# Optimization experiments

Hardware: AMD Instinct MI355X
Metric: run time of the kernel (lower is better)

The kernel has to match this reference:

```python
import jax, jax.numpy as jnp
import numpy as np

CONTEXT_LENGTH = 4096
INPUT_LENGTH = 1024
N_EMBED = 512
HEAD_SIZE = 64
BATCH = 8


def _prefix_causal_mask(T):
    # A=ones(IL,IL), B=zeros(IL,non), C=ones(non,IL), D=tril(non,non)
    il = INPUT_LENGTH
    non = CONTEXT_LENGTH - il
    top = jnp.concatenate([jnp.ones((il, il)), jnp.zeros((il, non))], axis=1)
    bot = jnp.concatenate([jnp.ones((non, il)), jnp.tril(jnp.ones((non, non)))], axis=1)
    E = jnp.concatenate([top, bot], axis=0)
    return E[:T, :T]


def setup_inputs() -> dict:
    key = jax.random.key(0)
    kx, kq, kk, kv = jax.random.split(key, 4)
    scale = N_EMBED ** -0.5
    return {
        "x": jax.random.normal(kx, (BATCH, CONTEXT_LENGTH, N_EMBED), dtype=jnp.float32),
        "Wq": jax.random.normal(kq, (N_EMBED, HEAD_SIZE), dtype=jnp.float32) * scale,
        "Wk": jax.random.normal(kk, (N_EMBED, HEAD_SIZE), dtype=jnp.float32) * scale,
        "Wv": jax.random.normal(kv, (N_EMBED, HEAD_SIZE), dtype=jnp.float32) * scale,
    }


def reference(x, Wq, Wk, Wv):
    B, T, C = x.shape
    q = x @ Wq  # [B,T,h]
    k = x @ Wk  # [B,T,h]
    v = x @ Wv  # [B,T,h]
    # NOTE: original scales by C**-0.5 with C = n_embed (not head_size)
    wei = jnp.einsum("bth,bsh->bts", q, k) * (C ** -0.5)  # [B,T,T]
    mask = _prefix_causal_mask(T)  # [T,T], 1 = visible
    wei = jnp.where(mask == 0, jnp.float32(-jnp.inf), wei)
    wei = jax.nn.softmax(wei, axis=-1)
    # dropout p=0.0 (eval): identity
    return jnp.einsum("bts,bsh->bth", wei, v)  # [B,T,h]
```

## Files before the change

### kernel.cpp

```cpp
#include <hip/hip_runtime.h>
#include <hip/hip_bf16.h>


typedef short short8 __attribute__((ext_vector_type(8)));
typedef float floatx4 __attribute__((ext_vector_type(4)));

static __device__ __forceinline__ unsigned short f2b(float f) {
  unsigned u = __float_as_uint(f);
  unsigned r = (u + 0x7fffu + ((u >> 16) & 1u)) >> 16;
  return (unsigned short)r;
}

static __device__ __forceinline__ unsigned pkbf(float lo, float hi) {
  __hip_bfloat162 t = __float22bfloat162_rn(make_float2(lo, hi));
  unsigned d;
  __builtin_memcpy(&d, &t, 4);
  return d;
}

union S8U {
  short8 s;
  unsigned u[4];
};

__global__ __launch_bounds__(256) void wtrans(
    const float* __restrict__ Wq, const float* __restrict__ Wk,
    const float* __restrict__ Wv, unsigned short* __restrict__ Wtf) {
  int o = blockIdx.x * 256 + threadIdx.x;
  int e = o & 7;
  int ln = (o >> 3) & 63;
  int jg = o >> 9;
  int ks = jg / 12;
  int j = jg % 12;
  int m = j >> 2;
  int n = (j & 3) * 16 + (ln & 15);
  int k = ks * 32 + (ln >> 4) * 8 + e;
  const float* W = (m == 0) ? Wq : (m == 1) ? Wk : Wv;
  Wtf[o] = f2b(W[k * 64 + n]);
}

__global__ __launch_bounds__(256, 3) void proj(
    const float* __restrict__ x, const unsigned short* __restrict__ Wtf,
    unsigned short* __restrict__ q, unsigned short* __restrict__ Kf,
    unsigned short* __restrict__ Vf) {
  __shared__ float Cc[2][12][16][17];

  const int tid = threadIdx.x;
  const int lane = tid & 63;
  const int w = tid >> 6;
  const int u = lane & 15;
  const int qd = lane >> 4;
  const int pr = w >> 1;
  const int p = w & 1;
  const int g0 = blockIdx.x * 32;

  floatx4 acc[12];
#pragma unroll
  for (int j = 0; j < 12; ++j) acc[j] = (floatx4)0.0f;

  const float* xr = x + (size_t)(g0 + pr * 16 + u) * 512;

  for (int it = 0; it < 8; ++it) {
    const int ks = p + it * 2;
    floatx4 x0 = *reinterpret_cast<const floatx4*>(&xr[ks * 32 + qd * 8]);
    floatx4 x1 = *reinterpret_cast<const floatx4*>(&xr[ks * 32 + qd * 8 + 4]);
    S8U a;
    a.u[0] = pkbf(x0[0], x0[1]);
    a.u[1] = pkbf(x0[2], x0[3]);
    a.u[2] = pkbf(x1[0], x1[1]);
    a.u[3] = pkbf(x1[2], x1[3]);
#pragma unroll
    for (int j = 0; j < 12; ++j) {
      short8 bfr = *reinterpret_cast<const short8*>(&Wtf[(size_t)(ks * 12 + j) * 512 + lane * 8]);
      acc[j] = __builtin_amdgcn_mfma_f32_16x16x32_bf16(a.s, bfr, acc[j], 0, 0, 0);
    }
  }

  if (p == 1) {
#pragma unroll
    for (int j = 0; j < 12; ++j)
#pragma unroll
      for (int r = 0; r < 4; ++r)
        Cc[pr][j][qd * 4 + r][u] = acc[j][r];
  }
  __syncthreads();
  if (p == 0) {
#pragma unroll
    for (int j = 0; j < 12; ++j)
#pragma unroll
      for (int r = 0; r < 4; ++r)
        acc[j][r] += Cc[pr][j][qd * 4 + r][u];

    const int rbase = g0 + pr * 16;
    const int b = rbase >> 12;
    const int t = rbase & 4095;
    const int kt = t >> 6;
    const int sb = ((blockIdx.x & 1) << 1) + pr;
    const int sp = blockIdx.x & 1;
    unsigned short* kfb = Kf + ((size_t)(b * 64 + kt)) * 4096;
    unsigned short* vfb = Vf + ((size_t)(b * 64 + kt)) * 4096;

#pragma unroll
    for (int j = 0; j < 4; ++j)
#pragma unroll
      for (int r = 0; r < 4; ++r) {
        q[(size_t)(rbase + qd * 4 + r) * 64 + j * 16 + u] = f2b(acc[j][r]);
        {
          int kh = j >> 1;
          int qd_f = ((j & 1) << 1) + (u >> 3);
          kfb[(size_t)(kh * 4 + sb) * 512 + (qd_f * 16 + (qd * 4 + r)) * 8 + (u & 7)] =
              f2b(acc[4 + j][r]);
        }
        {
          int qd_f = pr * 2 + (qd >> 1);
          int e = ((qd & 1) << 2) + r;
          vfb[(size_t)(sp * 4 + j) * 512 + (qd_f * 16 + u) * 8 + e] = f2b(acc[8 + j][r]);
        }
      }
  }
}

__global__ __launch_bounds__(256, 2) void attn(
    const unsigned short* __restrict__ q, const unsigned short* __restrict__ Kf,
    const unsigned short* __restrict__ Vf, float* __restrict__ out) {
  __shared__ unsigned Pb[4][4][64][4];
  __shared__ float OcA[64][68];
  __shared__ float OcB[64][68];
  __shared__ float Lc[4][64];

  const int tid = threadIdx.x;
  const int lane = tid & 63;
  const int w = tid >> 6;
  const int u = lane & 15;
  const int qd = lane >> 4;

  const int bx = blockIdx.x;
  const int b = bx & 7;
  const int i = bx >> 3;
  const int qt = (i < 32) ? i : (95 - i);
  const int g0 = qt * 64;

  const unsigned short* qp = q + (size_t)b * 4096 * 64;
  const unsigned short* kfp = Kf + (size_t)b * 64 * 4096;
  const unsigned short* vfp = Vf + (size_t)b * 64 * 4096;

  short8 qB[4][2];
#pragma unroll
  for (int nb = 0; nb < 4; ++nb)
#pragma unroll
    for (int kh = 0; kh < 2; ++kh)
      qB[nb][kh] = *reinterpret_cast<const short8*>(
          &qp[(size_t)(g0 + nb * 16 + u) * 64 + kh * 32 + qd * 8]);

  floatx4 OT[4][4];
#pragma unroll
  for (int mb = 0; mb < 4; ++mb)
#pragma unroll
    for (int nb = 0; nb < 4; ++nb) OT[mb][nb] = (floatx4)0.0f;
  float L[4] = {0.f, 0.f, 0.f, 0.f};

  const float cexp = 0.04419417382415922f * 1.4426950408889634f;
  const int ktmax = (qt < 16) ? 15 : qt;

  for (int kt = w; kt <= ktmax; kt += 4) {
    const unsigned short* kb = kfp + (size_t)kt * 4096;
    const unsigned short* vb = vfp + (size_t)kt * 4096;
    short8 kA[8];
#pragma unroll
    for (int f = 0; f < 8; ++f)
      kA[f] = *reinterpret_cast<const short8*>(&kb[(size_t)f * 512 + lane * 8]);
    const bool diag = (qt >= 16) && (kt == qt);

#pragma unroll
    for (int sp = 0; sp < 2; ++sp) {
      short8 vA[4];
#pragma unroll
      for (int mb = 0; mb < 4; ++mb)
        vA[mb] = *reinterpret_cast<const short8*>(
            &vb[(size_t)(sp * 4 + mb) * 512 + lane * 8]);

      floatx4 ST[2][4];
#pragma unroll
      for (int sbb = 0; sbb < 2; ++sbb)
#pragma unroll
        for (int nb = 0; nb < 4; ++nb) ST[sbb][nb] = (floatx4)0.0f;
#pragma unroll
      for (int kh = 0; kh < 2; ++kh)
#pragma unroll
        for (int sbb = 0; sbb < 2; ++sbb)
#pragma unroll
          for (int nb = 0; nb < 4; ++nb)
            ST[sbb][nb] = __builtin_amdgcn_mfma_f32_16x16x32_bf16(
                kA[kh * 4 + sp * 2 + sbb], qB[nb][kh], ST[sbb][nb], 0, 0, 0);

      if (diag) {
#pragma unroll
        for (int sbb = 0; sbb < 2; ++sbb)
#pragma unroll
          for (int nb = 0; nb < 4; ++nb)
#pragma unroll
            for (int r = 0; r < 4; ++r) {
              int sl = (sp * 2 + sbb) * 16 + qd * 4 + r;
              int qr = nb * 16 + u;
              if (sl > qr) ST[sbb][nb][r] = -__builtin_inff();
            }
      }

#pragma unroll
      for (int sbb = 0; sbb < 2; ++sbb)
#pragma unroll
        for (int nb = 0; nb < 4; ++nb) {
#pragma unroll
          for (int r = 0; r < 4; ++r)
            ST[sbb][nb][r] = __builtin_amdgcn_exp2f(ST[sbb][nb][r] * cexp);
          L[nb] += (ST[sbb][nb][0] + ST[sbb][nb][1]) + (ST[sbb][nb][2] + ST[sbb][nb][3]);
          unsigned lo = pkbf(ST[sbb][nb][0], ST[sbb][nb][1]);
          unsigned hi = pkbf(ST[sbb][nb][2], ST[sbb][nb][3]);
          int dl = (sbb * 2 + (qd >> 1)) * 16 + u;
          int d0 = (qd & 1) * 2;
          *reinterpret_cast<uint2*>(&Pb[w][nb][dl][d0]) = make_uint2(lo, hi);
        }

#pragma unroll
      for (int nb = 0; nb < 4; ++nb) {
        short8 pB = *reinterpret_cast<const short8*>(&Pb[w][nb][lane][0]);
#pragma unroll
        for (int mb = 0; mb < 4; ++mb)
          OT[mb][nb] = __builtin_amdgcn_mfma_f32_16x16x32_bf16(vA[mb], pB, OT[mb][nb], 0, 0, 0);
      }
    }
  }

#pragma unroll
  for (int nb = 0; nb < 4; ++nb) {
    L[nb] += __shfl_xor(L[nb], 16);
    L[nb] += __shfl_xor(L[nb], 32);
  }
  if (lane < 16) {
#pragma unroll
    for (int nb = 0; nb < 4; ++nb) Lc[w][nb * 16 + lane] = L[nb];
  }

  if (w == 1) {
#pragma unroll
    for (int mb = 0; mb < 4; ++mb)
#pragma unroll
      for (int nb = 0; nb < 4; ++nb)
        *reinterpret_cast<floatx4*>(&OcA[nb * 16 + u][mb * 16 + qd * 4]) = OT[mb][nb];
  }
  if (w == 3) {
#pragma unroll
    for (int mb = 0; mb < 4; ++mb)
#pragma unroll
      for (int nb = 0; nb < 4; ++nb)
        *reinterpret_cast<floatx4*>(&OcB[nb * 16 + u][mb * 16 + qd * 4]) = OT[mb][nb];
  }
  __syncthreads();
  if (w == 0) {
#pragma unroll
    for (int mb = 0; mb < 4; ++mb)
#pragma unroll
      for (int nb = 0; nb < 4; ++nb)
        OT[mb][nb] += *reinterpret_cast<const floatx4*>(&OcA[nb * 16 + u][mb * 16 + qd * 4]);
  }
  if (w == 2) {
#pragma unroll
    for (int mb = 0; mb < 4; ++mb)
#pragma unroll
      for (int nb = 0; nb < 4; ++nb) {
        OT[mb][nb] += *reinterpret_cast<const floatx4*>(&OcB[nb * 16 + u][mb * 16 + qd * 4]);
        *reinterpret_cast<floatx4*>(&OcB[nb * 16 + u][mb * 16 + qd * 4]) = OT[mb][nb];
      }
  }
  __syncthreads();
  if (w == 0) {
#pragma unroll
    for (int mb = 0; mb < 4; ++mb)
#pragma unroll
      for (int nb = 0; nb < 4; ++nb) {
        OT[mb][nb] += *reinterpret_cast<const floatx4*>(&OcB[nb * 16 + u][mb * 16 + qd * 4]);
        *reinterpret_cast<floatx4*>(&OcA[nb * 16 + u][mb * 16 + qd * 4]) = OT[mb][nb];
      }
  }
  __syncthreads();

  {
    int qr = tid >> 2;
    int h0 = (tid & 3) * 16;
    float Ltot = (Lc[0][qr] + Lc[1][qr]) + (Lc[2][qr] + Lc[3][qr]);
    float inv = 1.0f / Ltot;
    float* op = out + ((size_t)b * 4096 + g0 + qr) * 64 + h0;
#pragma unroll
    for (int c = 0; c < 4; ++c) {
      floatx4 v = *reinterpret_cast<const floatx4*>(&OcA[qr][h0 + c * 4]);
      v *= inv;
      *reinterpret_cast<floatx4*>(&op[c * 4]) = v;
    }
  }
}

extern "C" void kernel_launch(void* const* d_in, const int* in_sizes, int n_in,
                              void* d_out, int out_size, void* d_ws, size_t ws_size,
                              hipStream_t stream) {
  const float* x  = (const float*)d_in[0];
  const float* Wq = (const float*)d_in[1];
  const float* Wk = (const float*)d_in[2];
  const float* Wv = (const float*)d_in[3];

  unsigned short* ws = (unsigned short*)d_ws;
  unsigned short* Wtf = ws;
  unsigned short* qb = ws + 131072;
  unsigned short* kf = qb + 2097152;
  unsigned short* vf = kf + 2097152;

  wtrans<<<384, 256, 0, stream>>>(Wq, Wk, Wv, Wtf);
  proj<<<1024, 256, 0, stream>>>(x, Wtf, qb, kf, vf);
  attn<<<512, 256, 0, stream>>>(qb, kf, vf, (float*)d_out);
}
```

Before: 146.8 us.

## Split-K balance attention work across blocks with partial outputs and fold kernel

Replaces per-query-tile block assignment with a flat partition of all (query tile, key tile) work units so each block processes an equal number of key tiles, possibly spanning query-tile boundaries. Each block writes unnormalized partial outputs and row sums to workspace, and a new fold kernel sums the partials and normalizes. The softmax scale is also folded into q during projection, which removes a multiply per score. In exchange it adds an extra kernel launch and extra global traffic for the fp32 partials.

New measurement: 153.0 us. +4.3%, slower.

```diff
diff --git a/kernel.cpp b/kernel.cpp
--- a/kernel.cpp
+++ b/kernel.cpp
@@ -91,6 +91,7 @@
       for (int r = 0; r < 4; ++r)
         acc[j][r] += Cc[pr][j][qd * 4 + r][u];
 
+    const float cexp = 0.04419417382415922f * 1.4426950408889634f;
     const int rbase = g0 + pr * 16;
     const int b = rbase >> 12;
     const int t = rbase & 4095;
@@ -104,7 +105,7 @@
     for (int j = 0; j < 4; ++j)
 #pragma unroll
       for (int r = 0; r < 4; ++r) {
-        q[(size_t)(rbase + qd * 4 + r) * 64 + j * 16 + u] = f2b(acc[j][r]);
+        q[(size_t)(rbase + qd * 4 + r) * 64 + j * 16 + u] = f2b(acc[j][r] * cexp);
         {
           int kh = j >> 1;
           int qd_f = ((j & 1) << 1) + (u >> 3);
@@ -122,7 +123,8 @@
 
 __global__ __launch_bounds__(256, 2) void attn(
     const unsigned short* __restrict__ q, const unsigned short* __restrict__ Kf,
-    const unsigned short* __restrict__ Vf, float* __restrict__ out) {
+    const unsigned short* __restrict__ Vf, float* __restrict__ Op,
+    float* __restrict__ Lp) {
   __shared__ unsigned Pb[4][4][64][4];
   __shared__ float OcA[64][68];
   __shared__ float OcB[64][68];
@@ -136,166 +138,229 @@
 
   const int bx = blockIdx.x;
   const int b = bx & 7;
-  const int i = bx >> 3;
-  const int qt = (i < 32) ? i : (95 - i);
-  const int g0 = qt * 64;
+  const int s = bx >> 3;
+
+  const int ts = (s * 2200) >> 6;
+  const int te = ((s + 1) * 2200) >> 6;
 
   const unsigned short* qp = q + (size_t)b * 4096 * 64;
   const unsigned short* kfp = Kf + (size_t)b * 64 * 4096;
   const unsigned short* vfp = Vf + (size_t)b * 64 * 4096;
 
-  short8 qB[4][2];
-#pragma unroll
-  for (int nb = 0; nb < 4; ++nb)
-#pragma unroll
-    for (int kh = 0; kh < 2; ++kh)
-      qB[nb][kh] = *reinterpret_cast<const short8*>(
-          &qp[(size_t)(g0 + nb * 16 + u) * 64 + kh * 32 + qd * 8]);
-
-  floatx4 OT[4][4];
-#pragma unroll
-  for (int mb = 0; mb < 4; ++mb)
-#pragma unroll
-    for (int nb = 0; nb < 4; ++nb) OT[mb][nb] = (floatx4)0.0f;
-  float L[4] = {0.f, 0.f, 0.f, 0.f};
-
-  const float cexp = 0.04419417382415922f * 1.4426950408889634f;
-  const int ktmax = (qt < 16) ? 15 : qt;
-
-  for (int kt = w; kt <= ktmax; kt += 4) {
-    const unsigned short* kb = kfp + (size_t)kt * 4096;
-    const unsigned short* vb = vfp + (size_t)kt * 4096;
-    short8 kA[8];
-#pragma unroll
-    for (int f = 0; f < 8; ++f)
-      kA[f] = *reinterpret_cast<const short8*>(&kb[(size_t)f * 512 + lane * 8]);
-    const bool diag = (qt >= 16) && (kt == qt);
-
-#pragma unroll
-    for (int sp = 0; sp < 2; ++sp) {
-      short8 vA[4];
-#pragma unroll
-      for (int mb = 0; mb < 4; ++mb)
-        vA[mb] = *reinterpret_cast<const short8*>(
-            &vb[(size_t)(sp * 4 + mb) * 512 + lane * 8]);
-
-      floatx4 ST[2][4];
-#pragma unroll
-      for (int sbb = 0; sbb < 2; ++sbb)
-#pragma unroll
-        for (int nb = 0; nb < 4; ++nb) ST[sbb][nb] = (floatx4)0.0f;
+  int qt = 0, cq = 0;
+  while (cq + ((qt < 16) ? 16 : (qt + 1)) <= ts) {
+    cq += (qt < 16) ? 16 : (qt + 1);
+    ++qt;
+  }
+
+  int tcur = ts;
+  while (tcur < te) {
+    const int tq = (qt < 16) ? 16 : (qt + 1);
+    const int a = tcur - cq;
+    const int bnd = (tq < te - cq) ? tq : (te - cq);
+    int k0 = (cq * 64) / 2200;
+    while ((((k0 + 1) * 2200) >> 6) <= cq) ++k0;
+    const int o = s - k0;
+    const int g0 = qt * 64;
+    const int diagkt = (qt >= 16) ? qt : -1;
+
+    short8 qB[4][2];
+#pragma unroll
+    for (int nb = 0; nb < 4; ++nb)
 #pragma unroll
       for (int kh = 0; kh < 2; ++kh)
+        qB[nb][kh] = *reinterpret_cast<const short8*>(
+            &qp[(size_t)(g0 + nb * 16 + u) * 64 + kh * 32 + qd * 8]);
+
+    floatx4 OT[4][4];
+#pragma unroll
+    for (int mb = 0; mb < 4; ++mb)
+#pragma unroll
+      for (int nb = 0; nb < 4; ++nb) OT[mb][nb] = (floatx4)0.0f;
+    float L[4] = {0.f, 0.f, 0.f, 0.f};
+
+    for (int kt = a + w; kt < bnd; kt += 4) {
+      const unsigned short* kb = kfp + (size_t)kt * 4096;
+      const unsigned short* vb = vfp + (size_t)kt * 4096;
+      short8 kA[8];
+#pragma unroll
+      for (int f = 0; f < 8; ++f)
+        kA[f] = *reinterpret_cast<const short8*>(&kb[(size_t)f * 512 + lane * 8]);
+      const bool diag = (kt == diagkt);
+
+#pragma unroll
+      for (int sp = 0; sp < 2; ++sp) {
+        short8 vA[4];
+#pragma unroll
+        for (int mb = 0; mb < 4; ++mb)
+          vA[mb] = *reinterpret_cast<const short8*>(
+              &vb[(size_t)(sp * 4 + mb) * 512 + lane * 8]);
+
+        floatx4 ST[2][4];
 #pragma unroll
         for (int sbb = 0; sbb < 2; ++sbb)
 #pragma unroll
-          for (int nb = 0; nb < 4; ++nb)
-            ST[sbb][nb] = __builtin_amdgcn_mfma_f32_16x16x32_bf16(
-                kA[kh * 4 + sp * 2 + sbb], qB[nb][kh], ST[sbb][nb], 0, 0, 0);
-
-      if (diag) {
+          for (int nb = 0; nb < 4; ++nb) ST[sbb][nb] = (floatx4)0.0f;
+#pragma unroll
+        for (int kh = 0; kh < 2; ++kh)
+#pragma unroll
+          for (int sbb = 0; sbb < 2; ++sbb)
+#pragma unroll
+            for (int nb = 0; nb < 4; ++nb)
+              ST[sbb][nb] = __builtin_amdgcn_mfma_f32_16x16x32_bf16(
+                  kA[kh * 4 + sp * 2 + sbb], qB[nb][kh], ST[sbb][nb], 0, 0, 0);
+
+        if (diag) {
+#pragma unroll
+          for (int sbb = 0; sbb < 2; ++sbb)
+#pragma unroll
+            for (int nb = 0; nb < 4; ++nb)
+#pragma unroll
+              for (int r = 0; r < 4; ++r) {
+                int sl = (sp * 2 + sbb) * 16 + qd * 4 + r;
+                int qr = nb * 16 + u;
+                if (sl > qr) ST[sbb][nb][r] = -__builtin_inff();
+              }
+        }
+
 #pragma unroll
         for (int sbb = 0; sbb < 2; ++sbb)
 #pragma unroll
-          for (int nb = 0; nb < 4; ++nb)
-#pragma unroll
-            for (int r = 0; r < 4; ++r) {
-              int sl = (sp * 2 + sbb) * 16 + qd * 4 + r;
-              int qr = nb * 16 + u;
-              if (sl > qr) ST[sbb][nb][r] = -__builtin_inff();
-            }
+          for (int nb = 0; nb < 4; ++nb) {
+#pragma unroll
+            for (int r = 0; r < 4; ++r)
+              ST[sbb][nb][r] = __builtin_amdgcn_exp2f(ST[sbb][nb][r]);
+            L[nb] += (ST[sbb][nb][0] + ST[sbb][nb][1]) + (ST[sbb][nb][2] + ST[sbb][nb][3]);
+            unsigned lo = pkbf(ST[sbb][nb][0], ST[sbb][nb][1]);
+            unsigned hi = pkbf(ST[sbb][nb][2], ST[sbb][nb][3]);
+            int dl = (sbb * 2 + (qd >> 1)) * 16 + u;
+            int d0 = (qd & 1) * 2;
+            *reinterpret_cast<uint2*>(&Pb[w][nb][dl][d0]) = make_uint2(lo, hi);
+          }
+
+#pragma unroll
+        for (int nb = 0; nb < 4; ++nb) {
+          short8 pB = *reinterpret_cast<const short8*>(&Pb[w][nb][lane][0]);
+#pragma unroll
+          for (int mb = 0; mb < 4; ++mb)
+            OT[mb][nb] = __builtin_amdgcn_mfma_f32_16x16x32_bf16(vA[mb], pB, OT[mb][nb], 0, 0, 0);
+        }
       }
-
-#pragma unroll
-      for (int sbb = 0; sbb < 2; ++sbb)
+    }
+
+#pragma unroll
+    for (int nb = 0; nb < 4; ++nb) {
+      L[nb] += __shfl_xor(L[nb], 16);
+      L[nb] += __shfl_xor(L[nb], 32);
+    }
+    if (lane < 16) {
+#pragma unroll
+      for (int nb = 0; nb < 4; ++nb) Lc[w][nb * 16 + lane] = L[nb];
+    }
+
+    if (w == 1) {
+#pragma unroll
+      for (int mb = 0; mb < 4; ++mb)
+#pragma unroll
+        for (int nb = 0; nb < 4; ++nb)
+          *reinterpret_cast<floatx4*>(&OcA[nb * 16 + u][mb * 16 + qd * 4]) = OT[mb][nb];
+    }
+    if (w == 3) {
+#pragma unroll
+      for (int mb = 0; mb < 4; ++mb)
+#pragma unroll
+        for (int nb = 0; nb < 4; ++nb)
+          *reinterpret_cast<floatx4*>(&OcB[nb * 16 + u][mb * 16 + qd * 4]) = OT[mb][nb];
+    }
+    __syncthreads();
+    if (w == 0) {
+#pragma unroll
+      for (int mb = 0; mb < 4; ++mb)
+#pragma unroll
+        for (int nb = 0; nb < 4; ++nb)
+          OT[mb][nb] += *reinterpret_cast<const floatx4*>(&OcA[nb * 16 + u][mb * 16 + qd * 4]);
+    }
+    if (w == 2) {
+#pragma unroll
+      for (int mb = 0; mb < 4; ++mb)
 #pragma unroll
         for (int nb = 0; nb < 4; ++nb) {
-#pragma unroll
-          for (int r = 0; r < 4; ++r)
-            ST[sbb][nb][r] = __builtin_amdgcn_exp2f(ST[sbb][nb][r] * cexp);
-          L[nb] += (ST[sbb][nb][0] + ST[sbb][nb][1]) + (ST[sbb][nb][2] + ST[sbb][nb][3]);
-          unsigned lo = pkbf(ST[sbb][nb][0], ST[sbb][nb][1]);
-          unsigned hi = pkbf(ST[sbb][nb][2], ST[sbb][nb][3]);
-          int dl = (sbb * 2 + (qd >> 1)) * 16 + u;
-          int d0 = (qd & 1) * 2;
-          *reinterpret_cast<uint2*>(&Pb[w][nb][dl][d0]) = make_uint2(lo, hi);
-        }
-
-#pragma unroll
-      for (int nb = 0; nb < 4; ++nb) {
-        short8 pB = *reinterpret_cast<const short8*>(&Pb[w][nb][lane][0]);
-#pragma unroll
-        for (int mb = 0; mb < 4; ++mb)
-          OT[mb][nb] = __builtin_amdgcn_mfma_f32_16x16x32_bf16(vA[mb], pB, OT[mb][nb], 0, 0, 0);
+          OT[mb][nb] += *reinterpret_cast<const floatx4*>(&OcB[nb * 16 + u][mb * 16 + qd * 4]);
+          *reinterpret_cast<floatx4*>(&OcB[nb * 16 + u][mb * 16 + qd * 4]) = OT[mb][nb];
+        }
+    }
+    __syncthreads();
+    if (w == 0) {
+#pragma unroll
+      for (int mb = 0; mb < 4; ++mb)
+#pragma unroll
+        for (int nb = 0; nb < 4; ++nb) {
+          OT[mb][nb] += *reinterpret_cast<const floatx4*>(&OcB[nb * 16 + u][mb * 16 + qd * 4]);
+          *reinterpret_cast<floatx4*>(&OcA[nb * 16 + u][mb * 16 + qd * 4]) = OT[mb][nb];
+        }
+    }
+    __syncthreads();
+
+    {
+      int qr = tid >> 2;
+      int h0 = (tid & 3) * 16;
+      float* op = Op + ((size_t)((b * 64 + qt) * 3 + o)) * 4096 + qr * 64 + h0;
+#pragma unroll
+      for (int c = 0; c < 4; ++c)
+        *reinterpret_cast<floatx4*>(&op[c * 4]) =
+            *reinterpret_cast<const floatx4*>(&OcA[qr][h0 + c * 4]);
+      if ((tid & 3) == 0) {
+        float Ltot = (Lc[0][qr] + Lc[1][qr]) + (Lc[2][qr] + Lc[3][qr]);
+        Lp[((size_t)((b * 64 + qt) * 3 + o)) * 64 + qr] = Ltot;
       }
     }
-  }
-
-#pragma unroll
-  for (int nb = 0; nb < 4; ++nb) {
-    L[nb] += __shfl_xor(L[nb], 16);
-    L[nb] += __shfl_xor(L[nb], 32);
-  }
-  if (lane < 16) {
-#pragma unroll
-    for (int nb = 0; nb < 4; ++nb) Lc[w][nb * 16 + lane] = L[nb];
-  }
-
-  if (w == 1) {
-#pragma unroll
-    for (int mb = 0; mb < 4; ++mb)
-#pragma unroll
-      for (int nb = 0; nb < 4; ++nb)
-        *reinterpret_cast<floatx4*>(&OcA[nb * 16 + u][mb * 16 + qd * 4]) = OT[mb][nb];
-  }
-  if (w == 3) {
-#pragma unroll
-    for (int mb = 0; mb < 4; ++mb)
-#pragma unroll
-      for (int nb = 0; nb < 4; ++nb)
-        *reinterpret_cast<floatx4*>(&OcB[nb * 16 + u][mb * 16 + qd * 4]) = OT[mb][nb];
-  }
-  __syncthreads();
-  if (w == 0) {
-#pragma unroll
-    for (int mb = 0; mb < 4; ++mb)
-#pragma unroll
-      for (int nb = 0; nb < 4; ++nb)
-        OT[mb][nb] += *reinterpret_cast<const floatx4*>(&OcA[nb * 16 + u][mb * 16 + qd * 4]);
-  }
-  if (w == 2) {
-#pragma unroll
-    for (int mb = 0; mb < 4; ++mb)
-#pragma unroll
-      for (int nb = 0; nb < 4; ++nb) {
-        OT[mb][nb] += *reinterpret_cast<const floatx4*>(&OcB[nb * 16 + u][mb * 16 + qd * 4]);
-        *reinterpret_cast<floatx4*>(&OcB[nb * 16 + u][mb * 16 + qd * 4]) = OT[mb][nb];
-      }
-  }
-  __syncthreads();
-  if (w == 0) {
-#pragma unroll
-    for (int mb = 0; mb < 4; ++mb)
-#pragma unroll
-      for (int nb = 0; nb < 4; ++nb) {
-        OT[mb][nb] += *reinterpret_cast<const floatx4*>(&OcB[nb * 16 + u][mb * 16 + qd * 4]);
-        *reinterpret_cast<floatx4*>(&OcA[nb * 16 + u][mb * 16 + qd * 4]) = OT[mb][nb];
-      }
-  }
-  __syncthreads();
-
-  {
-    int qr = tid >> 2;
-    int h0 = (tid & 3) * 16;
-    float Ltot = (Lc[0][qr] + Lc[1][qr]) + (Lc[2][qr] + Lc[3][qr]);
-    float inv = 1.0f / Ltot;
-    float* op = out + ((size_t)b * 4096 + g0 + qr) * 64 + h0;
-#pragma unroll
-    for (int c = 0; c < 4; ++c) {
-      floatx4 v = *reinterpret_cast<const floatx4*>(&OcA[qr][h0 + c * 4]);
-      v *= inv;
-      *reinterpret_cast<floatx4*>(&op[c * 4]) = v;
-    }
+    __syncthreads();
+
+    tcur = cq + bnd;
+    if (bnd == tq) { cq += tq; ++qt; }
+  }
+}
+
+__global__ __launch_bounds__(256) void fold(
+    const float* __restrict__ Op, const float* __restrict__ Lp,
+    float* __restrict__ out) {
+  const int bx = blockIdx.x;
+  const int b = bx & 7;
+  const int qt = bx >> 3;
+  const int cq = (qt < 16) ? 16 * qt : 256 + ((17 + qt) * (qt - 16)) / 2;
+  const int tq = (qt < 16) ? 16 : (qt + 1);
+
+  int k0 = (cq * 64) / 2200;
+  while ((((k0 + 1) * 2200) >> 6) <= cq) ++k0;
+  const int last = cq + tq - 1;
+  int k1 = (last * 64) / 2200;
+  while ((((k1 + 1) * 2200) >> 6) <= last) ++k1;
+  const int n = k1 - k0 + 1;
+
+  const int t = threadIdx.x;
+  const int qr = t >> 2;
+  const int h0 = (t & 3) * 16;
+  const size_t pbase = (size_t)((b * 64 + qt) * 3);
+
+  float Ltot = 0.f;
+  for (int o = 0; o < n; ++o) Ltot += Lp[(pbase + o) * 64 + qr];
+
+  floatx4 acc[4];
+#pragma unroll
+  for (int c = 0; c < 4; ++c) acc[c] = (floatx4)0.0f;
+  for (int o = 0; o < n; ++o) {
+    const float* src = Op + (pbase + o) * 4096 + qr * 64 + h0;
+#pragma unroll
+    for (int c = 0; c < 4; ++c)
+      acc[c] += *reinterpret_cast<const floatx4*>(&src[c * 4]);
+  }
+
+  const float inv = 1.0f / Ltot;
+  float* op = out + ((size_t)(b * 4096 + qt * 64 + qr)) * 64 + h0;
+#pragma unroll
+  for (int c = 0; c < 4; ++c) {
+    floatx4 v = acc[c] * inv;
+    *reinterpret_cast<floatx4*>(&op[c * 4]) = v;
   }
 }
 
@@ -312,8 +377,11 @@
   unsigned short* qb = ws + 131072;
   unsigned short* kf = qb + 2097152;
   unsigned short* vf = kf + 2097152;
+  float* Op = (float*)(ws + 8388608);
+  float* Lp = Op + (size_t)8 * 64 * 3 * 4096;
 
   wtrans<<<384, 256, 0, stream>>>(Wq, Wk, Wv, Wtf);
   proj<<<1024, 256, 0, stream>>>(x, Wtf, qb, kf, vf);
-  attn<<<512, 256, 0, stream>>>(qb, kf, vf, (float*)d_out);
-}
+  attn<<<512, 256, 0, stream>>>(qb, kf, vf, Op, Lp);
+  fold<<<512, 256, 0, stream>>>(Op, Lp, (float*)d_out);
+}
```

## Prefetch next K tile via async global-to-LDS loads and fold softmax scale into Q

Applied to the files above, without the earlier changes.

The attention loop now issues async global_load_lds copies of the next K tile into a per-wave LDS buffer while the current tile is computed, then reads it back into registers at the end of the iteration. The buffer shares storage with the output-reduction scratch through a union. The softmax scale is also folded into Q in the projection kernel, which drops one multiply per score element. The risks are full vmcnt waits that also stall on the V loads, extra LDS round trips and traffic, and slightly different rounding because the scale is applied before the bf16 conversion.

Result: slower. 150.4 us (+2.5%).

```diff
diff --git a/kernel.cpp b/kernel.cpp
--- a/kernel.cpp
+++ b/kernel.cpp
@@ -22,6 +22,12 @@
   short8 s;
   unsigned u[4];
 };
+
+static __device__ __forceinline__ void gload_lds16(const void* g, void* l) {
+  __builtin_amdgcn_global_load_lds(
+      (const __attribute__((address_space(1))) unsigned int*)g,
+      (__attribute__((address_space(3))) unsigned int*)l, 16, 0, 0);
+}
 
 __global__ __launch_bounds__(256) void wtrans(
     const float* __restrict__ Wq, const float* __restrict__ Wk,
@@ -91,6 +97,7 @@
       for (int r = 0; r < 4; ++r)
         acc[j][r] += Cc[pr][j][qd * 4 + r][u];
 
+    const float cexp = 0.04419417382415922f * 1.4426950408889634f;
     const int rbase = g0 + pr * 16;
     const int b = rbase >> 12;
     const int t = rbase & 4095;
@@ -104,7 +111,7 @@
     for (int j = 0; j < 4; ++j)
 #pragma unroll
       for (int r = 0; r < 4; ++r) {
-        q[(size_t)(rbase + qd * 4 + r) * 64 + j * 16 + u] = f2b(acc[j][r]);
+        q[(size_t)(rbase + qd * 4 + r) * 64 + j * 16 + u] = f2b(acc[j][r] * cexp);
         {
           int kh = j >> 1;
           int qd_f = ((j & 1) << 1) + (u >> 3);
@@ -123,9 +130,15 @@
 __global__ __launch_bounds__(256, 2) void attn(
     const unsigned short* __restrict__ q, const unsigned short* __restrict__ Kf,
     const unsigned short* __restrict__ Vf, float* __restrict__ out) {
+  union SU {
+    unsigned short Kp[4][4096];
+    struct {
+      float OcA[64][68];
+      float OcB[64][68];
+    } oc;
+  };
+  __shared__ SU sh;
   __shared__ unsigned Pb[4][4][64][4];
-  __shared__ float OcA[64][68];
-  __shared__ float OcB[64][68];
   __shared__ float Lc[4][64];
 
   const int tid = threadIdx.x;
@@ -159,16 +172,30 @@
     for (int nb = 0; nb < 4; ++nb) OT[mb][nb] = (floatx4)0.0f;
   float L[4] = {0.f, 0.f, 0.f, 0.f};
 
-  const float cexp = 0.04419417382415922f * 1.4426950408889634f;
   const int ktmax = (qt < 16) ? 15 : qt;
 
+#define KDMA(SRC)                                                          \
+  do {                                                                     \
+    _Pragma("unroll")                                                      \
+    for (int f = 0; f < 8; ++f)                                            \
+      gload_lds16((SRC) + (size_t)f * 512 + lane * 8, &sh.Kp[w][f * 512]); \
+  } while (0)
+
+  short8 kA[8];
+  KDMA(kfp + (size_t)w * 4096);
+  asm volatile("s_waitcnt vmcnt(0)" ::: "memory");
+#pragma unroll
+  for (int f = 0; f < 8; ++f)
+    kA[f] = *reinterpret_cast<const short8*>(&sh.Kp[w][f * 512 + lane * 8]);
+
   for (int kt = w; kt <= ktmax; kt += 4) {
-    const unsigned short* kb = kfp + (size_t)kt * 4096;
+    const bool havenext = (kt + 4 <= ktmax);
+    if (havenext) {
+      asm volatile("s_waitcnt lgkmcnt(0)" ::: "memory");
+      KDMA(kfp + (size_t)(kt + 4) * 4096);
+    }
+
     const unsigned short* vb = vfp + (size_t)kt * 4096;
-    short8 kA[8];
-#pragma unroll
-    for (int f = 0; f < 8; ++f)
-      kA[f] = *reinterpret_cast<const short8*>(&kb[(size_t)f * 512 + lane * 8]);
     const bool diag = (qt >= 16) && (kt == qt);
 
 #pragma unroll
@@ -212,7 +239,7 @@
         for (int nb = 0; nb < 4; ++nb) {
 #pragma unroll
           for (int r = 0; r < 4; ++r)
-            ST[sbb][nb][r] = __builtin_amdgcn_exp2f(ST[sbb][nb][r] * cexp);
+            ST[sbb][nb][r] = __builtin_amdgcn_exp2f(ST[sbb][nb][r]);
           L[nb] += (ST[sbb][nb][0] + ST[sbb][nb][1]) + (ST[sbb][nb][2] + ST[sbb][nb][3]);
           unsigned lo = pkbf(ST[sbb][nb][0], ST[sbb][nb][1]);
           unsigned hi = pkbf(ST[sbb][nb][2], ST[sbb][nb][3]);
@@ -229,7 +256,17 @@
           OT[mb][nb] = __builtin_amdgcn_mfma_f32_16x16x32_bf16(vA[mb], pB, OT[mb][nb], 0, 0, 0);
       }
     }
-  }
+
+    if (havenext) {
+      asm volatile("s_waitcnt vmcnt(0)" ::: "memory");
+#pragma unroll
+      for (int f = 0; f < 8; ++f)
+        kA[f] = *reinterpret_cast<const short8*>(&sh.Kp[w][f * 512 + lane * 8]);
+    }
+  }
+#undef KDMA
+
+  __syncthreads();
 
 #pragma unroll
   for (int nb = 0; nb < 4; ++nb) {
@@ -246,14 +283,14 @@
     for (int mb = 0; mb < 4; ++mb)
 #pragma unroll
       for (int nb = 0; nb < 4; ++nb)
-        *reinterpret_cast<floatx4*>(&OcA[nb * 16 + u][mb * 16 + qd * 4]) = OT[mb][nb];
+        *reinterpret_cast<floatx4*>(&sh.oc.OcA[nb * 16 + u][mb * 16 + qd * 4]) = OT[mb][nb];
   }
   if (w == 3) {
 #pragma unroll
     for (int mb = 0; mb < 4; ++mb)
 #pragma unroll
       for (int nb = 0; nb < 4; ++nb)
-        *reinterpret_cast<floatx4*>(&OcB[nb * 16 + u][mb * 16 + qd * 4]) = OT[mb][nb];
+        *reinterpret_cast<floatx4*>(&sh.oc.OcB[nb * 16 + u][mb * 16 + qd * 4]) = OT[mb][nb];
   }
   __syncthreads();
   if (w == 0) {
@@ -261,15 +298,15 @@
     for (int mb = 0; mb < 4; ++mb)
 #pragma unroll
       for (int nb = 0; nb < 4; ++nb)
-        OT[mb][nb] += *reinterpret_cast<const floatx4*>(&OcA[nb * 16 + u][mb * 16 + qd * 4]);
+        OT[mb][nb] += *reinterpret_cast<const floatx4*>(&sh.oc.OcA[nb * 16 + u][mb * 16 + qd * 4]);
   }
   if (w == 2) {
 #pragma unroll
     for (int mb = 0; mb < 4; ++mb)
 #pragma unroll
       for (int nb = 0; nb < 4; ++nb) {
-        OT[mb][nb] += *reinterpret_cast<const floatx4*>(&OcB[nb * 16 + u][mb * 16 + qd * 4]);
-        *reinterpret_cast<floatx4*>(&OcB[nb * 16 + u][mb * 16 + qd * 4]) = OT[mb][nb];
+        OT[mb][nb] += *reinterpret_cast<const floatx4*>(&sh.oc.OcB[nb * 16 + u][mb * 16 + qd * 4]);
+        *reinterpret_cast<floatx4*>(&sh.oc.OcB[nb * 16 + u][mb * 16 + qd * 4]) = OT[mb][nb];
       }
   }
   __syncthreads();
@@ -278,8 +315,8 @@
     for (int mb = 0; mb < 4; ++mb)
 #pragma unroll
       for (int nb = 0; nb < 4; ++nb) {
-        OT[mb][nb] += *reinterpret_cast<const floatx4*>(&OcB[nb * 16 + u][mb * 16 + qd * 4]);
-        *reinterpret_cast<floatx4*>(&OcA[nb * 16 + u][mb * 16 + qd * 4]) = OT[mb][nb];
+        OT[mb][nb] += *reinterpret_cast<const floatx4*>(&sh.oc.OcB[nb * 16 + u][mb * 16 + qd * 4]);
+        *reinterpret_cast<floatx4*>(&sh.oc.OcA[nb * 16 + u][mb * 16 + qd * 4]) = OT[mb][nb];
       }
   }
   __syncthreads();
@@ -292,7 +329,7 @@
     float* op = out + ((size_t)b * 4096 + g0 + qr) * 64 + h0;
 #pragma unroll
     for (int c = 0; c < 4; ++c) {
-      floatx4 v = *reinterpret_cast<const floatx4*>(&OcA[qr][h0 + c * 4]);
+      floatx4 v = *reinterpret_cast<const floatx4*>(&sh.oc.OcA[qr][h0 + c * 4]);
       v *= inv;
       *reinterpret_cast<floatx4*>(&op[c * 4]) = v;
     }
```
